# Kernel optimization log

Measured on AMD Instinct MI355X. Metric: run time of the kernel, lower is better.

The kernel has to match this reference:

```python
import jax, jax.numpy as jnp
import numpy as np

N, F_IN, H, OUT, E = 50000, 128, 128, 40, 800000


def setup_inputs() -> dict:
    key = jax.random.key(0)
    ks = jax.random.split(key, 20)
    s = 0.05
    return {
        "x": jax.random.normal(ks[0], (N, F_IN), jnp.float32),
        "edge_index": jax.random.randint(ks[1], (2, E), 0, N, jnp.int64),
        # GATConv (heads=1)
        "W_gat": jax.random.normal(ks[2], (F_IN, H), jnp.float32) * s,
        "att_src": jax.random.normal(ks[3], (H,), jnp.float32) * s,
        "att_dst": jax.random.normal(ks[4], (H,), jnp.float32) * s,
        "b_gat": jnp.zeros((H,), jnp.float32),
        # GCNConv
        "W_gcn": jax.random.normal(ks[5], (F_IN, H), jnp.float32) * s,
        "b_gcn": jnp.zeros((H,), jnp.float32),
        # SAGEConv (mean aggr): lin_l on neighbors (with bias), lin_r on root (no bias)
        "W_sage_l": jax.random.normal(ks[6], (F_IN, H), jnp.float32) * s,
        "b_sage_l": jnp.zeros((H,), jnp.float32),
        "W_sage_r": jax.random.normal(ks[7], (F_IN, H), jnp.float32) * s,
        # MLP head
        "W1": jax.random.normal(ks[8], (3 * H, 2 * H), jnp.float32) * s,
        "b1": jnp.zeros((2 * H,), jnp.float32),
        "W2": jax.random.normal(ks[9], (2 * H, H), jnp.float32) * s,
        "b2": jnp.zeros((H,), jnp.float32),
        "W3": jax.random.normal(ks[10], (H, OUT), jnp.float32) * s,
        "b3": jnp.zeros((OUT,), jnp.float32),
        # BatchNorm1d(3H)
        "gamma": jnp.ones((3 * H,), jnp.float32),
        "beta": jnp.zeros((3 * H,), jnp.float32),
    }


def _add_self_loops(edge_index, n):
    loop = jnp.arange(n, dtype=edge_index.dtype)
    src = jnp.concatenate([edge_index[0], loop])
    dst = jnp.concatenate([edge_index[1], loop])
    return src, dst


def _gat(x, src, dst, n, W, att_src, att_dst, bias):
    h = x @ W                                   # [N, H]
    a_s = h @ att_src                           # [N]
    a_d = h @ att_dst                           # [N]
    e = jax.nn.leaky_relu(a_s[src] + a_d[dst], 0.2)  # [E']
    m = jax.ops.segment_max(e, dst, num_segments=n)
    ex = jnp.exp(e - m[dst])
    denom = jax.ops.segment_sum(ex, dst, num_segments=n)
    alpha = ex / denom[dst]
    out = jax.ops.segment_sum(alpha[:, None] * h[src], dst, num_segments=n)
    return out + bias


def _gcn(x, src, dst, n, W, bias):
    h = x @ W
    deg = jax.ops.segment_sum(jnp.ones_like(dst, dtype=h.dtype), dst, num_segments=n)
    dinv = jnp.where(deg > 0, jax.lax.rsqrt(deg), 0.0)
    norm = dinv[src] * dinv[dst]                # [E']
    out = jax.ops.segment_sum(norm[:, None] * h[src], dst, num_segments=n)
    return out + bias


def _sage(x, src, dst, n, W_l, b_l, W_r):
    agg = jax.ops.segment_sum(x[src], dst, num_segments=n)
    cnt = jax.ops.segment_sum(jnp.ones_like(dst, dtype=x.dtype), dst, num_segments=n)
    mean = agg / jnp.maximum(cnt, 1.0)[:, None]
    return mean @ W_l + b_l + x @ W_r


def reference(x, edge_index, W_gat, att_src, att_dst, b_gat, W_gcn, b_gcn,
              W_sage_l, b_sage_l, W_sage_r, W1, b1, W2, b2, W3, b3, gamma, beta):
    n = x.shape[0]
    src, dst = edge_index[0], edge_index[1]          # SAGE: no self-loops
    src_sl, dst_sl = _add_self_loops(edge_index, n)  # GAT/GCN add self-loops

    x_gat = _gat(x, src_sl, dst_sl, n, W_gat, att_src, att_dst, b_gat)
    x_gcn = _gcn(x, src_sl, dst_sl, n, W_gcn, b_gcn)
    x_sage = _sage(x, src, dst, n, W_sage_l, b_sage_l, W_sage_r)

    h = jnp.concatenate([x_gat, x_gcn, x_sage], axis=1)  # [N, 3H]
    # BatchNorm1d (training-mode batch statistics; biased variance, eps=1e-5)
    mu = h.mean(axis=0)
    var = h.var(axis=0)
    h = (h - mu) * jax.lax.rsqrt(var + 1e-5) * gamma + beta
    # dropout is identity at inference
    h = jax.nn.relu(h) @ W1 + b1
    h = jax.nn.relu(h) @ W2 + b2
    h = jax.nn.relu(h) @ W3 + b3
    return h
```

## Files before the change

kernel.cpp:

```cpp
#include <hip/hip_runtime.h>
#include <cstdint>
#include <cstddef>

#define NN   50000
#define FIN  128
#define HD   128
#define EE   800000
#define C3   384
#define NOUT 40

#define NBLK ((NN + 127) / 128)

#define NBUCK ((NN + 511) / 512)
#define BCAP  16384
#define BK_BLKS ((EE + 8191) / 8192)
#define SCAP  12288
#define SXB   ((NN + 16) / 16)

#define RCAP      132
#define STORE_CAP 128
#define ZROW NN

#define LDSW 132
#define A2W  136

typedef __attribute__((ext_vector_type(8))) short s8v;
typedef __attribute__((ext_vector_type(4))) float f4v;
typedef __attribute__((ext_vector_type(8))) ushort u8v;

typedef const __attribute__((address_space(1))) unsigned int* guintp;
typedef __attribute__((address_space(3))) unsigned int* luintp;

static __device__ __forceinline__ void async_copy16(const void* g, void* l) {
    __builtin_amdgcn_global_load_lds((guintp)g, (luintp)l, 16, 0, 0);
}

static __device__ __forceinline__ float b2f(ushort u) {
    return __uint_as_float((unsigned)u << 16);
}
static __device__ __forceinline__ ushort f2b(float v) {
    unsigned u = __float_as_uint(v);
    unsigned r = u + 0x7fffu + ((u >> 16) & 1u);
    return (ushort)(r >> 16);
}

__global__ __launch_bounds__(1024) void k_bucketw(
    const int* __restrict__ e_src, const int* __restrict__ e_dst,
    int* __restrict__ bcnt, uint* __restrict__ ebuf,
    const float* __restrict__ Wg, const float* __restrict__ Wc,
    const float* __restrict__ Wl, const float* __restrict__ Wr,
    const float* __restrict__ W1, const float* __restrict__ W2,
    const float* __restrict__ W3,
    const float* __restrict__ asv, const float* __restrict__ adv,
    float* __restrict__ w_as, float* __restrict__ w_ad,
    ushort* __restrict__ btg, ushort* __restrict__ btc,
    ushort* __restrict__ btsg,
    ushort* __restrict__ bt1, ushort* __restrict__ bt2,
    ushort* __restrict__ bt3)
{
    int t = threadIdx.x;
    if (blockIdx.x >= BK_BLKS) {
        int ry = blockIdx.x - BK_BLKS;
        if (ry == 816) {
            if (t < 128) {
                float s1 = 0.f, s2 = 0.f;
                for (int j = 0; j < 128; ++j) {
                    float w = Wg[t * 128 + j];
                    s1 += w * asv[j];
                    s2 += w * adv[j];
                }
                w_as[t] = s1; w_ad[t] = s2;
            }
            return;
        }
        const float* W = nullptr; ushort* dh; int K, Nw, n;
        bool sage = false;
        if (ry < 128)      { n = ry;       K = 128; Nw = 128; W = Wg; dh = btg; }
        else if (ry < 256) { n = ry - 128; K = 128; Nw = 128; W = Wc; dh = btc; }
        else if (ry < 384) { n = ry - 256; K = 256; Nw = 128; sage = true; dh = btsg; }
        else if (ry < 640) { n = ry - 384; K = 384; Nw = 256; W = W1; dh = bt1; }
        else if (ry < 768) { n = ry - 640; K = 256; Nw = 128; W = W2; dh = bt2; }
        else               { n = ry - 768; K = 128; Nw = 40;  W = W3; dh = bt3; }
        for (int k = t; k < K; k += 1024) {
            float v;
            if (sage) v = (k < 128) ? Wl[(size_t)k * 128 + n] : Wr[(size_t)(k - 128) * 128 + n];
            else      v = (n < Nw) ? W[(size_t)k * Nw + n] : 0.f;
            dh[(size_t)n * K + k] = f2b(v);
        }
        return;
    }
    __shared__ uint sval[8192];
    __shared__ int scnt[NBUCK], sbase[NBUCK];
    if (t < NBUCK) scnt[t] = 0;
    __syncthreads();
    int e0 = blockIdx.x * 8192;
    #pragma unroll
    for (int i = 0; i < 8; ++i) {
        int g = e0 + i * 1024 + t;
        uint val = 0xffffffffu;
        if (g < EE) {
            int d = e_dst[g];
            int s = e_src[g];
            int b = d >> 9;
            val = ((uint)b << 25) | ((uint)(d & 511) << 16) | (uint)s;
            atomicAdd(&scnt[b], 1);
        }
        sval[i * 1024 + t] = val;
    }
    __syncthreads();
    if (t < NBUCK) {
        sbase[t] = atomicAdd(&bcnt[t], scnt[t]);
        scnt[t] = 0;
    }
    __syncthreads();
    #pragma unroll
    for (int i = 0; i < 8; ++i) {
        uint val = sval[i * 1024 + t];
        if (val != 0xffffffffu) {
            int b = val >> 25;
            int lo = atomicAdd(&scnt[b], 1);
            ebuf[(size_t)b * BCAP + sbase[b] + lo] = val;
        }
    }
}

__global__ __launch_bounds__(1024) void k_csrx(
    const int* __restrict__ bcnt, const uint* __restrict__ ebuf,
    int* __restrict__ offs, float* __restrict__ dinv,
    ushort* __restrict__ esrc,
    const float* __restrict__ x,
    const float* __restrict__ w_as, const float* __restrict__ w_ad,
    ushort* __restrict__ xb, float* __restrict__ a_s, float* __restrict__ a_d)
{
    int t = threadIdx.x;
    if (blockIdx.x >= NBUCK) {
        int node = (blockIdx.x - NBUCK) * 16 + (t >> 6);
        if (node > NN) return;
        int lane = t & 63;
        size_t o = (size_t)node * 128 + lane * 2;
        if (node == NN) {
            ushort2 z; z.x = 0; z.y = 0;
            *(ushort2*)(xb + o) = z;
            return;
        }
        float2 v  = *(const float2*)(x + o);
        { ushort2 u; u.x = f2b(v.x); u.y = f2b(v.y); *(ushort2*)(xb + o) = u; }
        float2 w1 = *(const float2*)(w_as + lane * 2);
        float2 w2 = *(const float2*)(w_ad + lane * 2);
        float s1 = v.x * w1.x + v.y * w1.y;
        float s2 = v.x * w2.x + v.y * w2.y;
        #pragma unroll
        for (int off = 32; off; off >>= 1) {
            s1 += __shfl_down(s1, off);
            s2 += __shfl_down(s2, off);
        }
        if (lane == 0) { a_s[node] = s1; a_d[node] = s2; }
        return;
    }
    __shared__ ushort sout[SCAP];
    __shared__ int hist[512];
    __shared__ int sh[256];
    __shared__ int btop_s;
    int b = blockIdx.x;
    int d0 = b * 512;
    int ndst = NN - d0; if (ndst > 512) ndst = 512;
    if (t < 512) hist[t] = 0;
    __syncthreads();
    int nb = bcnt[b];
    const uint* eb = ebuf + (size_t)b * BCAP;
    for (int i = t; i < nb; i += 1024)
        atomicAdd(&hist[(eb[i] >> 16) & 511], 1);
    __syncthreads();
    if (t < 64) {
        int acc = 0;
        for (int i = t; i < b; i += 64) {
            int nd = NN - i * 512; if (nd > 512) nd = 512;
            acc += bcnt[i] + nd;
        }
        #pragma unroll
        for (int off = 32; off; off >>= 1) acc += __shfl_down(acc, off);
        if (t == 0) btop_s = acc;
    }
    int v0 = 0, v1 = 0;
    if (t < 256) {
        int i0g = d0 + t * 2;
        v0 = (i0g < NN) ? hist[t * 2] + 1 : 0;
        v1 = (i0g + 1 < NN) ? hist[t * 2 + 1] + 1 : 0;
        sh[t] = v0 + v1;
    }
    __syncthreads();
    for (int off = 1; off < 256; off <<= 1) {
        int u = 0;
        if (t < 256 && t >= off) u = sh[t - off];
        __syncthreads();
        if (t < 256) sh[t] += u;
        __syncthreads();
    }
    if (t < 256) {
        int pair = v0 + v1;
        int lex = sh[t] - pair;
        int excl = lex + btop_s;
        int i0g = d0 + t * 2;
        if (i0g < NN) {
            offs[i0g] = excl; dinv[i0g] = rsqrtf((float)v0);
            hist[t * 2] = lex;
        }
        if (i0g + 1 < NN) {
            offs[i0g + 1] = excl + v0; dinv[i0g + 1] = rsqrtf((float)v1);
            hist[t * 2 + 1] = lex + v0;
        }
        if (b == NBUCK - 1 && t == 255) offs[NN] = excl + pair;
    }
    __syncthreads();
    for (int i = t; i < nb; i += 1024) {
        uint val = eb[i];
        int slot = atomicAdd(&hist[(val >> 16) & 511], 1);
        sout[slot] = (ushort)(val & 0xffffu);
    }
    if (t < ndst) {
        int slot = atomicAdd(&hist[t], 1);
        sout[slot] = (ushort)(d0 + t);
    }
    __syncthreads();
    int total = nb + ndst;
    int obase = btop_s;
    for (int i = t; i < total; i += 1024)
        esrc[obase + i] = sout[i];
}

__global__ __launch_bounds__(256) void k_gather(
    const ushort* __restrict__ esrc, const int* __restrict__ offs,
    const float* __restrict__ a_s, const float* __restrict__ a_d,
    const float* __restrict__ dinv,
    const ushort* __restrict__ xb,
    ushort* __restrict__ tgb, ushort* __restrict__ tcb,
    ushort* __restrict__ tsb)
{
    __shared__ uint2 recs[16][RCAP];
    int t = threadIdx.x;
    int qid = t >> 4;
    int ln = t & 15;
    int d = blockIdx.x * 16 + qid;
    if (d >= NN) return;
    uint2* rec = recs[qid];
    int beg = offs[d], end = offs[d + 1];
    int cnt = end - beg;
    float ad = a_d[d], dd = dinv[d];
    int stored = cnt < STORE_CAP ? cnt : STORE_CAP;

    float mloc = -3.0e38f;
    for (int b = 0; b < cnt; b += 16) {
        int j = b + ln;
        if (j < cnt) {
            int s = esrc[beg + j];
            float e = a_s[s] + ad;
            e = (e > 0.f) ? e : 0.2f * e;
            mloc = fmaxf(mloc, e);
            if (j < STORE_CAP) {
                uint2 r;
                r.x = __float_as_uint(e);
                r.y = (uint)s | ((uint)f2b(dinv[s] * dd) << 16);
                rec[j] = r;
            }
        }
    }
    float m = mloc;
    #pragma unroll
    for (int off = 1; off < 16; off <<= 1) m = fmaxf(m, __shfl_xor(m, off, 16));

    float denl = 0.f;
    for (int j = ln; j < stored; j += 16) {
        float ex = expf(__uint_as_float(rec[j].x) - m);
        denl += ex;
        rec[j].x = __float_as_uint(ex);
    }
    for (int idx = beg + STORE_CAP + ln; idx < end; idx += 16) {
        int s = esrc[idx];
        float e = a_s[s] + ad;
        e = (e > 0.f) ? e : 0.2f * e;
        denl += expf(e - m);
    }
    float den = denl;
    #pragma unroll
    for (int off = 1; off < 16; off <<= 1) den += __shfl_xor(den, off, 16);
    float rden = 1.f / den;

    for (int j = ln; j < stored; j += 16) {
        uint2 r = rec[j];
        uint2 q;
        q.x = (uint)f2b(__uint_as_float(r.x) * rden) | (r.y & 0xffff0000u);
        q.y = r.y & 0xffffu;
        rec[j] = q;
    }
    if (ln < 2) { uint2 q; q.x = 0u; q.y = (uint)ZROW; rec[stored + ln] = q; }

    float tg[8] = {}, tc[8] = {}, ts[8] = {};
    const ushort* xbs = xb + ln * 8;
    auto ldx = [&](uint srow) -> u8v {
        return *(const u8v*)(xbs + (size_t)srow * 128);
    };
    auto fmacc = [&](u8v x8, uint pw) {
        float wg = __uint_as_float(pw << 16);
        float wc = __uint_as_float(pw & 0xffff0000u);
        #pragma unroll
        for (int k = 0; k < 8; ++k) {
            float xv = b2f(x8[k]);
            tg[k] += wg * xv;
            tc[k] += wc * xv;
            ts[k] += xv;
        }
    };

    int Pcnt = (stored + 1) & ~1;
    uint2 rA = rec[0]; u8v xA = ldx(rA.y);
    uint2 rB; u8v xB;
    int j = 0;
    for (;;) {
        rB = rec[j + 1]; xB = ldx(rB.y);
        fmacc(xA, rA.x);
        if (++j >= Pcnt) break;
        rA = rec[j + 1]; xA = ldx(rA.y);
        fmacc(xB, rB.x);
        if (++j >= Pcnt) break;
    }

    for (int base = beg + STORE_CAP; base < end; base += 16) {
        int idx = base + ln;
        int s = ZROW; uint pw = 0;
        if (idx < end) {
            int ss = esrc[idx];
            float e = a_s[ss] + ad;
            e = (e > 0.f) ? e : 0.2f * e;
            pw = (uint)f2b(expf(e - m) * rden) | ((uint)f2b(dinv[ss] * dd) << 16);
            s = ss;
        }
        int cb = end - base; if (cb > 16) cb = 16;
        for (int jj = 0; jj < cb; ++jj) {
            int sa = __shfl(s, jj, 16);
            uint pa = (uint)__shfl((int)pw, jj, 16);
            fmacc(ldx((uint)sa), pa);
        }
    }

    u8v xd = *(const u8v*)(xb + (size_t)d * 128 + ln * 8);
    int cs = cnt - 1;
    float rc = 1.f / (float)(cs > 1 ? cs : 1);
    u8v og, oc, os;
    #pragma unroll
    for (int k = 0; k < 8; ++k) {
        og[k] = f2b(tg[k]);
        oc[k] = f2b(tc[k]);
        os[k] = f2b((ts[k] - b2f(xd[k])) * rc);
    }
    size_t row = (size_t)d * 128 + ln * 8;
    *(u8v*)(tgb + row) = og;
    *(u8v*)(tcb + row) = oc;
    *(u8v*)(tsb + row) = os;
}

__global__ __launch_bounds__(256, 3) void k_gemm_prod(
    const ushort* __restrict__ tgb, const ushort* __restrict__ tcb,
    const ushort* __restrict__ tsb, const ushort* __restrict__ xb,
    const ushort* __restrict__ btg, const ushort* __restrict__ btc,
    const ushort* __restrict__ btsg,
    const float* __restrict__ bg, const float* __restrict__ bc,
    const float* __restrict__ bsl,
    float* __restrict__ pS, float* __restrict__ pQ,
    ushort* __restrict__ hch)
{
    constexpr int COLS = 128;
    constexpr int HOPU = 8 * COLS;
    __shared__ __align__(16) ushort S[16384];
    ushort* Bs = S;
    ushort* As = S + 8192;
    float* red = (float*)(S + 14336);

    const int z = blockIdx.z;
    const ushort* A1 = (z == 0) ? tgb : (z == 1) ? tcb : tsb;
    const ushort* Bt = (z == 0) ? btg : (z == 1) ? btc : btsg;
    const float*  bias = (z == 0) ? bg : (z == 1) ? bc : bsl;
    const int nch = (z == 2) ? 2 : 1;
    const int ktot = nch * 128;

    const int lane = threadIdx.x & 63;
    const int wave = threadIdx.x >> 6;
    const int quad = lane >> 4;
    const int ln15 = lane & 15;
    const int row0 = blockIdx.x * 128 + wave * 32;
    const int Rbase = blockIdx.x * 128;

    auto stageB = [&](int c, int h) {
        for (int u0 = wave * 64; u0 < HOPU; u0 += 256) {
            int u  = u0 + lane;
            int kq  = u / COLS;
            int col = u - kq * COLS;
            int kk  = c * 128 + h * 64 + kq * 8;
            const ushort* gp = Bt + (size_t)col * ktot + kk;
            async_copy16(gp, (char*)Bs + (size_t)u0 * 16);
        }
    };
    auto stageA = [&](int c, int h) {
        #pragma unroll
        for (int i = 0; i < 4; ++i) {
            int u0 = (wave * 4 + i) * 64;
            int u  = u0 + lane;
            int row = u >> 3;
            int s   = u & 7;
            int sg  = s ^ (row & 7);
            int rr = Rbase + row; if (rr > NN - 1) rr = NN - 1;
            int kk = c * 128 + h * 64 + sg * 8;
            const ushort* gp = (kk < 128) ? (A1 + (size_t)rr * 128 + kk)
                                          : (xb + (size_t)rr * 128 + (kk - 128));
            async_copy16(gp, (char*)As + (size_t)u0 * 16);
        }
    };
    auto afrag = [&](int jj, int mt) -> s8v {
        int r = wave * 32 + mt * 16 + ln15;
        int sg = jj * 4 + quad;
        int unit = r * 8 + (sg ^ (r & 7));
        return *(const s8v*)(As + (size_t)unit * 8);
    };

    f4v acc[2][8] = {};

    auto compute = [&](int jj) {
        s8v a0 = afrag(jj, 0);
        s8v a1 = afrag(jj, 1);
        #pragma unroll
        for (int t = 0; t < 8; ++t) {
            int ub = (jj * 4 + quad) * COLS + t * 16 + ln15;
            s8v b = *(const s8v*)(Bs + (size_t)ub * 8);
            acc[0][t] = __builtin_amdgcn_mfma_f32_16x16x32_bf16(a0, b, acc[0][t], 0, 0, 0);
            acc[1][t] = __builtin_amdgcn_mfma_f32_16x16x32_bf16(a1, b, acc[1][t], 0, 0, 0);
        }
    };

    stageB(0, 0); stageA(0, 0);
    __syncthreads();

    for (int ph = 0; ph < nch; ++ph) {
        for (int h = 0; h < 2; ++h) {
            compute(0); compute(1);
            if (!(ph == nch - 1 && h == 1)) {
                __syncthreads();
                int nc = ph, nh = h + 1;
                if (nh == 2) { nh = 0; ++nc; }
                stageB(nc, nh); stageA(nc, nh);
                __syncthreads();
            }
        }
    }

    __syncthreads();
    if (threadIdx.x < 256) red[threadIdx.x] = 0.f;
    ushort* Lp = S + wave * 2176;
    float sp[8] = {}, qp[8] = {};
    #pragma unroll
    for (int mt = 0; mt < 2; ++mt) {
        #pragma unroll
        for (int t = 0; t < 8; ++t) {
            #pragma unroll
            for (int r = 0; r < 4; ++r) {
                int rr = row0 + mt * 16 + quad * 4 + r;
                float v = acc[mt][t][r] + bias[t * 16 + ln15];
                Lp[(quad * 4 + r) * LDSW + t * 16 + ln15] = f2b(v);
                if (rr < NN) { sp[t] += v; qp[t] += v * v; }
            }
        }
        int cb = (lane & 31) * 4;
        #pragma unroll
        for (int it = 0; it < 8; ++it) {
            int row2 = it * 2 + (lane >> 5);
            int rr = row0 + mt * 16 + row2;
            uint2 v = *(uint2*)(Lp + row2 * LDSW + cb);
            if (rr < NN)
                *(uint2*)(hch + (size_t)rr * C3 + z * 128 + cb) = v;
        }
    }
    __syncthreads();
    #pragma unroll
    for (int t = 0; t < 8; ++t) {
        float s = sp[t], q = qp[t];
        s += __shfl_xor(s, 16); s += __shfl_xor(s, 32);
        q += __shfl_xor(q, 16); q += __shfl_xor(q, 32);
        if (quad == 0) {
            atomicAdd(&red[t * 16 + ln15], s);
            atomicAdd(&red[128 + t * 16 + ln15], q);
        }
    }
    __syncthreads();
    if (threadIdx.x < 128) {
        size_t o = (size_t)blockIdx.x * C3 + z * 128 + threadIdx.x;
        pS[o] = red[threadIdx.x];
        pQ[o] = red[128 + threadIdx.x];
    }
}

__global__ void k_bn_final(const float* __restrict__ pS, const float* __restrict__ pQ,
                           const float* __restrict__ gamma, const float* __restrict__ beta,
                           float* __restrict__ scale, float* __restrict__ shift)
{
    int t = threadIdx.x;
    int j = blockIdx.x * 64 + (t >> 2);
    int part = t & 3;
    if (j >= C3) return;
    float s = 0.f, q = 0.f;
    for (int r = part; r < NBLK; r += 4) {
        s += pS[(size_t)r * C3 + j];
        q += pQ[(size_t)r * C3 + j];
    }
    s += __shfl_down(s, 2); s += __shfl_down(s, 1);
    q += __shfl_down(q, 2); q += __shfl_down(q, 1);
    if (part == 0) {
        const float rn = 1.f / (float)NN;
        float mu  = s * rn;
        float var = q * rn - mu * mu;
        float sc  = gamma[j] * rsqrtf(var + 1e-5f);
        scale[j] = sc;
        shift[j] = beta[j] - mu * sc;
    }
}

template<int NT, int NCH, int AX, int BN>
__global__ __launch_bounds__(256, BN ? 4 : 5) void k_gemm2(
    const ushort* __restrict__ A, int K,
    const ushort* __restrict__ Bt,
    int M, int mode,
    const float* __restrict__ bias,
    float* __restrict__ Cf, int ldc,
    ushort* __restrict__ Ch, int ldch,
    int colmax,
    const float* __restrict__ bnscale, const float* __restrict__ bnshift)
{
    constexpr int COLS = NT * 16;
    constexpr int HOPU = 8 * COLS;
    constexpr int KTOT = NCH * 128;

    __shared__ __align__(16) ushort S[16384];
    __shared__ float bns[BN ? 768 : 4];
    ushort* Bs = S;
    ushort* As = S + 8192;

    const int lane = threadIdx.x & 63;
    const int wave = threadIdx.x >> 6;
    const int quad = lane >> 4;
    const int ln15 = lane & 15;
    const int brow = AX ? blockIdx.y : blockIdx.x;
    const int bcol = AX ? blockIdx.x : blockIdx.y;
    const int row0 = brow * 128 + wave * 32;
    const int col0 = bcol * COLS;
    const int Rbase = brow * 128;

    auto stageB = [&](int c, int h) {
        for (int u0 = wave * 64; u0 < HOPU; u0 += 256) {
            int u  = u0 + lane;
            int kq  = u / COLS;
            int col = u - kq * COLS;
            int kk  = c * 128 + h * 64 + kq * 8;
            const ushort* gp = Bt + (size_t)(col0 + col) * KTOT + kk;
            async_copy16(gp, (char*)Bs + (size_t)u0 * 16);
        }
    };
    auto stageA = [&](int c, int h) {
        #pragma unroll
        for (int i = 0; i < 4; ++i) {
            int u0 = (wave * 4 + i) * 64;
            int u  = u0 + lane;
            int row = u >> 3;
            int s   = u & 7;
            int sg  = s ^ (row & 7);
            int rr = Rbase + row; if (rr > M - 1) rr = M - 1;
            int kk = c * 128 + h * 64 + sg * 8;
            const ushort* gp = A + (size_t)rr * K + kk;
            async_copy16(gp, (char*)As + (size_t)u0 * 16);
        }
    };
    auto afrag = [&](int jj, int mt) -> s8v {
        int r = wave * 32 + mt * 16 + ln15;
        int sg = jj * 4 + quad;
        int unit = r * 8 + (sg ^ (r & 7));
        return *(const s8v*)(As + (size_t)unit * 8);
    };

    f4v acc[2][NT] = {};

    auto compute = [&](int jj, int kk0) {
        s8v a0 = afrag(jj, 0);
        s8v a1 = afrag(jj, 1);
        if constexpr (BN) {
            int cb0 = kk0 + (jj * 4 + quad) * 8;
            #pragma unroll
            for (int e = 0; e < 8; ++e) {
                float sc = bns[cb0 + e];
                float sh = bns[384 + cb0 + e];
                float v0 = b2f((ushort)a0[e]) * sc + sh;
                float v1 = b2f((ushort)a1[e]) * sc + sh;
                v0 = v0 > 0.f ? v0 : 0.f;
                v1 = v1 > 0.f ? v1 : 0.f;
                a0[e] = (short)f2b(v0);
                a1[e] = (short)f2b(v1);
            }
        }
        #pragma unroll
        for (int t = 0; t < NT; ++t) {
            int ub = (jj * 4 + quad) * COLS + t * 16 + ln15;
            s8v b = *(const s8v*)(Bs + (size_t)ub * 8);
            acc[0][t] = __builtin_amdgcn_mfma_f32_16x16x32_bf16(a0, b, acc[0][t], 0, 0, 0);
            acc[1][t] = __builtin_amdgcn_mfma_f32_16x16x32_bf16(a1, b, acc[1][t], 0, 0, 0);
        }
    };

    if constexpr (BN) {
        for (int j = threadIdx.x; j < 384; j += 256) {
            bns[j] = bnscale[j];
            bns[384 + j] = bnshift[j];
        }
    }
    stageB(0, 0); stageA(0, 0);
    __syncthreads();

    #pragma unroll
    for (int ph = 0; ph < NCH; ++ph) {
        #pragma unroll
        for (int h = 0; h < 2; ++h) {
            int kk0 = ph * 128 + h * 64;
            compute(0, kk0); compute(1, kk0);
            if (!(ph == NCH - 1 && h == 1)) {
                __syncthreads();
                int nc = ph, nh = h + 1;
                if (nh == 2) { nh = 0; ++nc; }
                stageB(nc, nh); stageA(nc, nh);
                __syncthreads();
            }
        }
    }

    if (NT == 8 && mode == 0) {
        __syncthreads();
        ushort* Lp = S + wave * 2176;
        #pragma unroll
        for (int mt = 0; mt < 2; ++mt) {
            #pragma unroll
            for (int t = 0; t < NT; ++t) {
                int cc = col0 + t * 16 + ln15;
                #pragma unroll
                for (int r = 0; r < 4; ++r) {
                    float v = acc[mt][t][r] + bias[cc];
                    v = v > 0.f ? v : 0.f;
                    Lp[(quad * 4 + r) * LDSW + t * 16 + ln15] = f2b(v);
                }
            }
            int cb = (lane & 31) * 4;
            #pragma unroll
            for (int it = 0; it < 8; ++it) {
                int row2 = it * 2 + (lane >> 5);
                int rr = row0 + mt * 16 + row2;
                uint2 v = *(uint2*)(Lp + row2 * LDSW + cb);
                if (rr < M)
                    *(uint2*)(Ch + (size_t)rr * ldch + col0 + cb) = v;
            }
        }
    } else {
        #pragma unroll
        for (int t = 0; t < NT; ++t) {
            int cc = col0 + t * 16 + ln15;
            #pragma unroll
            for (int mt = 0; mt < 2; ++mt) {
                #pragma unroll
                for (int r = 0; r < 4; ++r) {
                    int rr = row0 + mt * 16 + quad * 4 + r;
                    if (rr < M && cc < colmax)
                        Cf[(size_t)rr * ldc + cc] = acc[mt][t][r] + bias[cc];
                }
            }
        }
    }
}

__global__ __launch_bounds__(256, 2) void k_gemm23(
    const ushort* __restrict__ A,
    const ushort* __restrict__ Bt2, const ushort* __restrict__ Bt3,
    const float* __restrict__ b2v, const float* __restrict__ b3v,
    float* __restrict__ out)
{
    constexpr int COLS = 128;
    constexpr int HOPU = 1024;
    constexpr int KTOT = 256;
    __shared__ __align__(16) ushort S[16384];
    __shared__ __align__(16) ushort A2[128 * A2W];
    ushort* Bs = S;
    ushort* As = S + 8192;

    const int lane = threadIdx.x & 63;
    const int wave = threadIdx.x >> 6;
    const int quad = lane >> 4;
    const int ln15 = lane & 15;
    const int Rbase = blockIdx.x * 128;
    const int row0 = Rbase + wave * 32;

    auto stageB = [&](int c, int h) {
        for (int u0 = wave * 64; u0 < HOPU; u0 += 256) {
            int u  = u0 + lane;
            int kq  = u / COLS;
            int col = u - kq * COLS;
            int kk  = c * 128 + h * 64 + kq * 8;
            async_copy16(Bt2 + (size_t)col * KTOT + kk, (char*)Bs + (size_t)u0 * 16);
        }
    };
    auto stageA = [&](int c, int h) {
        #pragma unroll
        for (int i = 0; i < 4; ++i) {
            int u0 = (wave * 4 + i) * 64;
            int u  = u0 + lane;
            int row = u >> 3;
            int s   = u & 7;
            int sg  = s ^ (row & 7);
            int rr = Rbase + row; if (rr > NN - 1) rr = NN - 1;
            int kk = c * 128 + h * 64 + sg * 8;
            async_copy16(A + (size_t)rr * KTOT + kk, (char*)As + (size_t)u0 * 16);
        }
    };
    auto afrag = [&](int jj, int mt) -> s8v {
        int r = wave * 32 + mt * 16 + ln15;
        int sg = jj * 4 + quad;
        int unit = r * 8 + (sg ^ (r & 7));
        return *(const s8v*)(As + (size_t)unit * 8);
    };

    f4v acc[2][8] = {};
    auto compute = [&](int jj) {
        s8v a0 = afrag(jj, 0);
        s8v a1 = afrag(jj, 1);
        #pragma unroll
        for (int t = 0; t < 8; ++t) {
            int ub = (jj * 4 + quad) * COLS + t * 16 + ln15;
            s8v b = *(const s8v*)(Bs + (size_t)ub * 8);
            acc[0][t] = __builtin_amdgcn_mfma_f32_16x16x32_bf16(a0, b, acc[0][t], 0, 0, 0);
            acc[1][t] = __builtin_amdgcn_mfma_f32_16x16x32_bf16(a1, b, acc[1][t], 0, 0, 0);
        }
    };

    stageB(0, 0); stageA(0, 0);
    __syncthreads();
    #pragma unroll
    for (int ph = 0; ph < 2; ++ph) {
        #pragma unroll
        for (int h = 0; h < 2; ++h) {
            compute(0); compute(1);
            if (!(ph == 1 && h == 1)) {
                __syncthreads();
                int nc = ph, nh = h + 1;
                if (nh == 2) { nh = 0; ++nc; }
                stageB(nc, nh); stageA(nc, nh);
                __syncthreads();
            }
        }
    }

    __syncthreads();
    for (int u0 = wave * 64; u0 < 768; u0 += 256) {
        int u = u0 + lane;
        int h = u / 384;
        int rem = u - h * 384;
        int kq = rem / 48;
        int col = rem - kq * 48;
        int kk = h * 64 + kq * 8;
        async_copy16(Bt3 + (size_t)col * 128 + kk, (char*)S + (size_t)u0 * 16);
    }
    #pragma unroll
    for (int mt = 0; mt < 2; ++mt) {
        #pragma unroll
        for (int t = 0; t < 8; ++t) {
            int cc = t * 16 + ln15;
            float bb = b2v[cc];
            #pragma unroll
            for (int r = 0; r < 4; ++r) {
                int rl = wave * 32 + mt * 16 + quad * 4 + r;
                float v = acc[mt][t][r] + bb;
                v = v > 0.f ? v : 0.f;
                A2[(size_t)rl * A2W + cc] = f2b(v);
            }
        }
    }
    __syncthreads();

    f4v acc3[2][3] = {};
    #pragma unroll
    for (int h = 0; h < 2; ++h) {
        #pragma unroll
        for (int jj = 0; jj < 2; ++jj) {
            int sg = jj * 4 + quad;
            int ko = h * 64 + sg * 8;
            s8v a0 = *(const s8v*)(A2 + (size_t)(wave * 32 + ln15) * A2W + ko);
            s8v a1 = *(const s8v*)(A2 + (size_t)(wave * 32 + 16 + ln15) * A2W + ko);
            #pragma unroll
            for (int t = 0; t < 3; ++t) {
                int ub = h * 384 + sg * 48 + t * 16 + ln15;
                s8v b = *(const s8v*)(S + (size_t)ub * 8);
                acc3[0][t] = __builtin_amdgcn_mfma_f32_16x16x32_bf16(a0, b, acc3[0][t], 0, 0, 0);
                acc3[1][t] = __builtin_amdgcn_mfma_f32_16x16x32_bf16(a1, b, acc3[1][t], 0, 0, 0);
            }
        }
    }
    #pragma unroll
    for (int t = 0; t < 3; ++t) {
        int cc = t * 16 + ln15;
        #pragma unroll
        for (int mt = 0; mt < 2; ++mt) {
            #pragma unroll
            for (int r = 0; r < 4; ++r) {
                int rr = row0 + mt * 16 + quad * 4 + r;
                if (rr < NN && cc < NOUT)
                    out[(size_t)rr * NOUT + cc] = acc3[mt][t][r] + b3v[cc];
            }
        }
    }
}

extern "C" void kernel_launch(void* const* d_in, const int* in_sizes, int n_in,
                              void* d_out, int out_size, void* d_ws, size_t ws_size,
                              hipStream_t stream) {
    const float* x        = (const float*)d_in[0];
    const int*   ei       = (const int*)d_in[1];
    const float* W_gat    = (const float*)d_in[2];
    const float* att_src  = (const float*)d_in[3];
    const float* att_dst  = (const float*)d_in[4];
    const float* b_gat    = (const float*)d_in[5];
    const float* W_gcn    = (const float*)d_in[6];
    const float* b_gcn    = (const float*)d_in[7];
    const float* W_sage_l = (const float*)d_in[8];
    const float* b_sage_l = (const float*)d_in[9];
    const float* W_sage_r = (const float*)d_in[10];
    const float* W1       = (const float*)d_in[11];
    const float* b1       = (const float*)d_in[12];
    const float* W2       = (const float*)d_in[13];
    const float* b2       = (const float*)d_in[14];
    const float* W3       = (const float*)d_in[15];
    const float* b3       = (const float*)d_in[16];
    const float* gamma    = (const float*)d_in[17];
    const float* beta     = (const float*)d_in[18];

    const int* e_src = ei;
    const int* e_dst = ei + EE;

    char* base = (char*)d_ws;
    size_t o = 0;
    ushort* hch  = (ushort*)(base + o); o += (size_t)NN * C3 * 2;
    ushort* tgb  = (ushort*)(base + o); o += (size_t)NN * 128 * 2;
    ushort* tcb  = (ushort*)(base + o); o += (size_t)NN * 128 * 2;
    ushort* tsb  = (ushort*)(base + o); o += (size_t)NN * 128 * 2;
    ushort* xb   = (ushort*)(base + o); o += (size_t)(NN + 1) * 128 * 2;
    ushort* esrc = (ushort*)(base + o); o += ((size_t)(EE + NN) * 2 + 15) & ~15ull;
    int*    offs = (int*)(base + o);    o += (size_t)(NN + 16) * 4;
    float*  as_  = (float*)(base + o);  o += (size_t)NN * 4;
    float*  ad_  = (float*)(base + o);  o += (size_t)NN * 4;
    float*  dinv = (float*)(base + o);  o += (size_t)NN * 4;
    int*    bcnt = (int*)(base + o);    o += 128 * 4;
    float*  pS   = (float*)(base + o);  o += (size_t)NBLK * C3 * 4;
    float*  pQ   = (float*)(base + o);  o += (size_t)NBLK * C3 * 4;
    float*  scale= (float*)(base + o);  o += C3 * 4;
    float*  shift= (float*)(base + o);  o += C3 * 4;
    float*  w_as = (float*)(base + o);  o += 128 * 4;
    float*  w_ad = (float*)(base + o);  o += 128 * 4;
    ushort* btg  = (ushort*)(base + o); o += 128 * 128 * 2;
    ushort* btc  = (ushort*)(base + o); o += 128 * 128 * 2;
    ushort* btsg = (ushort*)(base + o); o += 128 * 256 * 2;
    ushort* bt1  = (ushort*)(base + o); o += 256 * 384 * 2;
    ushort* bt2  = (ushort*)(base + o); o += 128 * 256 * 2;
    ushort* bt3  = (ushort*)(base + o); o += 48 * 128 * 2;
    ushort* a1 = tgb;
    uint*   ebuf = (uint*)hch;

    hipMemsetAsync(bcnt, 0, 128 * 4, stream);

    k_bucketw<<<BK_BLKS + 817, 1024, 0, stream>>>(
        e_src, e_dst, bcnt, ebuf,
        W_gat, W_gcn, W_sage_l, W_sage_r, W1, W2, W3,
        att_src, att_dst, w_as, w_ad, btg, btc, btsg, bt1, bt2, bt3);

    k_csrx<<<NBUCK + SXB, 1024, 0, stream>>>(
        bcnt, ebuf, offs, dinv, esrc,
        x, w_as, w_ad, xb, as_, ad_);

    k_gather<<<(NN + 15) / 16, 256, 0, stream>>>(
        esrc, offs, as_, ad_, dinv, xb, tgb, tcb, tsb);

    k_gemm_prod<<<dim3(NBLK, 1, 3), 256, 0, stream>>>(
        tgb, tcb, tsb, xb, btg, btc, btsg,
        b_gat, b_gcn, b_sage_l, pS, pQ, hch);

    k_bn_final<<<6, 256, 0, stream>>>(pS, pQ, gamma, beta, scale, shift);

    k_gemm2<8, 3, 1, 1><<<dim3(2, NBLK), 256, 0, stream>>>(
        hch, 384, bt1, NN, 0, b1, nullptr, 0, a1, 256, 256, scale, shift);

    k_gemm23<<<NBLK, 256, 0, stream>>>(a1, bt2, bt3, b2, b3, (float*)d_out);
}
```

Before: 271.4 us.

## Compute full 256-column MLP1 tile per block with shared BN pre-pass

The templated GEMM that split the 256 output columns across two blocks is replaced by a dedicated kernel where each block computes all 256 columns for its 128 rows. The A tile is therefore loaded once instead of twice. BatchNorm scale/shift plus ReLU is applied once in LDS by a cooperative pass rather than per-wave on every fragment, which removes duplicated conversion work. In exchange the kernel uses more LDS and accumulator registers, dropping occupancy to 2 blocks per CU, launches half as many blocks, and adds an extra barrier per k-step.

```diff
diff --git a/kernel.cpp b/kernel.cpp
--- a/kernel.cpp
+++ b/kernel.cpp
@@ -521,44 +521,35 @@
     }
 }
 
-template<int NT, int NCH, int AX, int BN>
-__global__ __launch_bounds__(256, BN ? 4 : 5) void k_gemm2(
-    const ushort* __restrict__ A, int K,
+__global__ __launch_bounds__(256, 2) void k_gemm1(
+    const ushort* __restrict__ A,
     const ushort* __restrict__ Bt,
-    int M, int mode,
     const float* __restrict__ bias,
-    float* __restrict__ Cf, int ldc,
-    ushort* __restrict__ Ch, int ldch,
-    int colmax,
+    ushort* __restrict__ Ch,
     const float* __restrict__ bnscale, const float* __restrict__ bnshift)
 {
-    constexpr int COLS = NT * 16;
-    constexpr int HOPU = 8 * COLS;
-    constexpr int KTOT = NCH * 128;
-
-    __shared__ __align__(16) ushort S[16384];
-    __shared__ float bns[BN ? 768 : 4];
+    __shared__ __align__(16) ushort S[24576];
+    __shared__ float bns[768];
     ushort* Bs = S;
-    ushort* As = S + 8192;
+    ushort* As = S + 16384;
 
     const int lane = threadIdx.x & 63;
     const int wave = threadIdx.x >> 6;
     const int quad = lane >> 4;
     const int ln15 = lane & 15;
-    const int brow = AX ? blockIdx.y : blockIdx.x;
-    const int bcol = AX ? blockIdx.x : blockIdx.y;
-    const int row0 = brow * 128 + wave * 32;
-    const int col0 = bcol * COLS;
-    const int Rbase = brow * 128;
+    const int Rbase = blockIdx.x * 128;
+    const int row0 = Rbase + wave * 32;
 
     auto stageB = [&](int c, int h) {
-        for (int u0 = wave * 64; u0 < HOPU; u0 += 256) {
-            int u  = u0 + lane;
-            int kq  = u / COLS;
-            int col = u - kq * COLS;
+        for (int u0 = wave * 64; u0 < 2048; u0 += 256) {
+            int u   = u0 + lane;
+            int chh = u >> 10;
+            int rem = u & 1023;
+            int kq  = rem >> 7;
+            int col = rem & 127;
             int kk  = c * 128 + h * 64 + kq * 8;
-            const ushort* gp = Bt + (size_t)(col0 + col) * KTOT + kk;
-            async_copy16(gp, (char*)Bs + (size_t)u0 * 16);
+            async_copy16(Bt + (size_t)(chh * 128 + col) * 384 + kk,
+                         (char*)Bs + (size_t)u0 * 16);
         }
     };
     auto stageA = [&](int c, int h) {
@@ -569,10 +560,9 @@
             int row = u >> 3;
             int s   = u & 7;
             int sg  = s ^ (row & 7);
-            int rr = Rbase + row; if (rr > M - 1) rr = M - 1;
+            int rr = Rbase + row; if (rr > NN - 1) rr = NN - 1;
             int kk = c * 128 + h * 64 + sg * 8;
-            const ushort* gp = A + (size_t)rr * K + kk;
-            async_copy16(gp, (char*)As + (size_t)u0 * 16);
+            async_copy16(A + (size_t)rr * 384 + kk, (char*)As + (size_t)u0 * 16);
         }
     };
     auto afrag = [&](int jj, int mt) -> s8v {
@@ -581,51 +571,54 @@
         int unit = r * 8 + (sg ^ (r & 7));
         return *(const s8v*)(As + (size_t)unit * 8);
     };
-
-    f4v acc[2][NT] = {};
-
-    auto compute = [&](int jj, int kk0) {
+    auto bnpass = [&](int kk0) {
+        #pragma unroll
+        for (int i = 0; i < 4; ++i) {
+            int u = threadIdx.x + i * 256;
+            int sg = (u & 7) ^ ((u >> 3) & 7);
+            int c0 = kk0 + sg * 8;
+            u8v x8 = *(u8v*)(As + (size_t)u * 8);
+            #pragma unroll
+            for (int e = 0; e < 8; ++e) {
+                float v = b2f(x8[e]) * bns[c0 + e] + bns[384 + c0 + e];
+                v = v > 0.f ? v : 0.f;
+                x8[e] = f2b(v);
+            }
+            *(u8v*)(As + (size_t)u * 8) = x8;
+        }
+    };
+
+    f4v acc[2][2][8] = {};
+    auto compute = [&](int jj) {
         s8v a0 = afrag(jj, 0);
         s8v a1 = afrag(jj, 1);
-        if constexpr (BN) {
-            int cb0 = kk0 + (jj * 4 + quad) * 8;
+        #pragma unroll
+        for (int chh = 0; chh < 2; ++chh) {
             #pragma unroll
-            for (int e = 0; e < 8; ++e) {
-                float sc = bns[cb0 + e];
-                float sh = bns[384 + cb0 + e];
-                float v0 = b2f((ushort)a0[e]) * sc + sh;
-                float v1 = b2f((ushort)a1[e]) * sc + sh;
-                v0 = v0 > 0.f ? v0 : 0.f;
-                v1 = v1 > 0.f ? v1 : 0.f;
-                a0[e] = (short)f2b(v0);
-                a1[e] = (short)f2b(v1);
-            }
-        }
-        #pragma unroll
-        for (int t = 0; t < NT; ++t) {
-            int ub = (jj * 4 + quad) * COLS + t * 16 + ln15;
-            s8v b = *(const s8v*)(Bs + (size_t)ub * 8);
-            acc[0][t] = __builtin_amdgcn_mfma_f32_16x16x32_bf16(a0, b, acc[0][t], 0, 0, 0);
-            acc[1][t] = __builtin_amdgcn_mfma_f32_16x16x32_bf16(a1, b, acc[1][t], 0, 0, 0);
-        }
-    };
-
-    if constexpr (BN) {
-        for (int j = threadIdx.x; j < 384; j += 256) {
-            bns[j] = bnscale[j];
-            bns[384 + j] = bnshift[j];
-        }
+            for (int t = 0; t < 8; ++t) {
+                int ub = chh * 1024 + (jj * 4 + quad) * 128 + t * 16 + ln15;
+                s8v b = *(const s8v*)(Bs + (size_t)ub * 8);
+                acc[chh][0][t] = __builtin_amdgcn_mfma_f32_16x16x32_bf16(a0, b, acc[chh][0][t], 0, 0, 0);
+                acc[chh][1][t] = __builtin_amdgcn_mfma_f32_16x16x32_bf16(a1, b, acc[chh][1][t], 0, 0, 0);
+            }
+        }
+    };
+
+    for (int j = threadIdx.x; j < 384; j += 256) {
+        bns[j] = bnscale[j];
+        bns[384 + j] = bnshift[j];
     }
     stageB(0, 0); stageA(0, 0);
     __syncthreads();
 
     #pragma unroll
-    for (int ph = 0; ph < NCH; ++ph) {
+    for (int ph = 0; ph < 3; ++ph) {
         #pragma unroll
         for (int h = 0; h < 2; ++h) {
-            int kk0 = ph * 128 + h * 64;
-            compute(0, kk0); compute(1, kk0);
-            if (!(ph == NCH - 1 && h == 1)) {
+            bnpass(ph * 128 + h * 64);
+            __syncthreads();
+            compute(0); compute(1);
+            if (!(ph == 2 && h == 1)) {
                 __syncthreads();
                 int nc = ph, nh = h + 1;
                 if (nh == 2) { nh = 0; ++nc; }
@@ -635,17 +628,19 @@
         }
     }
 
-    if (NT == 8 && mode == 0) {
-        __syncthreads();
-        ushort* Lp = S + wave * 2176;
+    __syncthreads();
+    ushort* Lp = S + wave * 2176;
+    #pragma unroll
+    for (int chh = 0; chh < 2; ++chh) {
+        int col0 = chh * 128;
         #pragma unroll
         for (int mt = 0; mt < 2; ++mt) {
             #pragma unroll
-            for (int t = 0; t < NT; ++t) {
+            for (int t = 0; t < 8; ++t) {
                 int cc = col0 + t * 16 + ln15;
                 #pragma unroll
                 for (int r = 0; r < 4; ++r) {
-                    float v = acc[mt][t][r] + bias[cc];
+                    float v = acc[chh][mt][t][r] + bias[cc];
                     v = v > 0.f ? v : 0.f;
                     Lp[(quad * 4 + r) * LDSW + t * 16 + ln15] = f2b(v);
                 }
@@ -656,22 +651,8 @@
                 int row2 = it * 2 + (lane >> 5);
                 int rr = row0 + mt * 16 + row2;
                 uint2 v = *(uint2*)(Lp + row2 * LDSW + cb);
-                if (rr < M)
-                    *(uint2*)(Ch + (size_t)rr * ldch + col0 + cb) = v;
-            }
-        }
-    } else {
-        #pragma unroll
-        for (int t = 0; t < NT; ++t) {
-            int cc = col0 + t * 16 + ln15;
-            #pragma unroll
-            for (int mt = 0; mt < 2; ++mt) {
-                #pragma unroll
-                for (int r = 0; r < 4; ++r) {
-                    int rr = row0 + mt * 16 + quad * 4 + r;
-                    if (rr < M && cc < colmax)
-                        Cf[(size_t)rr * ldc + cc] = acc[mt][t][r] + bias[cc];
-                }
+                if (rr < NN)
+                    *(uint2*)(Ch + (size_t)rr * 256 + col0 + cb) = v;
             }
         }
     }
@@ -891,8 +872,7 @@
 
     k_bn_final<<<6, 256, 0, stream>>>(pS, pQ, gamma, beta, scale, shift);
 
-    k_gemm2<8, 3, 1, 1><<<dim3(2, NBLK), 256, 0, stream>>>(
-        hch, 384, bt1, NN, 0, b1, nullptr, 0, a1, 256, 256, scale, shift);
+    k_gemm1<<<NBLK, 256, 0, stream>>>(hch, bt1, b1, a1, scale, shift);
 
     k_gemm23<<<NBLK, 256, 0, stream>>>(a1, bt2, bt3, b2, b3, (float*)d_out);
 }
```

New measurement: 276.6 us. Within noise of the previous version (+1.9%).
